# Optimization experiments

Measured on AMD Instinct MI355X. Metric: run time of the kernel, lower is better.

Reference implementation:

```python
import jax, jax.numpy as jnp
import numpy as np

V, S, D, H, L = 32000, 2048, 768, 12, 6
HD = D // H
EPS = 1e-5


def _sinusoidal_pe(s, d):
    pos = np.arange(s)[:, None].astype(np.float32)
    div = np.exp(np.arange(0, d, 2).astype(np.float32) * (-np.log(10000.0) / d))
    pe = np.zeros((s, d), dtype=np.float32)
    pe[:, 0::2] = np.sin(pos * div)
    pe[:, 1::2] = np.cos(pos * div)
    return jnp.asarray(pe)


def setup_inputs() -> dict:
    key = jax.random.key(0)
    ks = jax.random.split(key, 16)
    std = 0.02
    tok_emb = jax.random.normal(ks[0], (V, D), jnp.float32) * std
    tok_emb = tok_emb.at[1].set(0.0)  # padding_idx=1
    pos_enc = _sinusoidal_pe(S, D)
    attn_w = jax.random.normal(ks[1], (L, 3 * D, D), jnp.float32) * std
    attn_b = jnp.zeros((L, 3 * D), jnp.float32)
    proj_std = 0.02 / np.sqrt(2 * 6)
    proj_w = jax.random.normal(ks[2], (L, D, D), jnp.float32) * proj_std
    proj_b = jnp.zeros((L, D), jnp.float32)
    ln1_g = jnp.ones((L, D), jnp.float32); ln1_b = jnp.zeros((L, D), jnp.float32)
    ln2_g = jnp.ones((L, D), jnp.float32); ln2_b = jnp.zeros((L, D), jnp.float32)
    fc1_w = jax.random.normal(ks[3], (L, 4 * D, D), jnp.float32) * std
    fc1_b = jnp.zeros((L, 4 * D), jnp.float32)
    fc2_w = jax.random.normal(ks[4], (L, D, 4 * D), jnp.float32) * std
    fc2_b = jnp.zeros((L, D), jnp.float32)
    dec_w = jax.random.normal(ks[5], (V, D), jnp.float32) * std
    idx = jax.random.randint(ks[6], (2, S), 0, V)
    return dict(idx=idx, tok_emb=tok_emb, pos_enc=pos_enc, attn_w=attn_w,
                attn_b=attn_b, proj_w=proj_w, proj_b=proj_b, ln1_g=ln1_g,
                ln1_b=ln1_b, ln2_g=ln2_g, ln2_b=ln2_b, fc1_w=fc1_w,
                fc1_b=fc1_b, fc2_w=fc2_w, fc2_b=fc2_b, dec_w=dec_w)


def _ln(x, g, b):
    mu = jnp.mean(x, -1, keepdims=True)
    var = jnp.mean(jnp.square(x - mu), -1, keepdims=True)
    return (x - mu) * jax.lax.rsqrt(var + EPS) * g + b


def _forward(idx, tok_emb, pos_enc, attn_w, attn_b, proj_w, proj_b,
             ln1_g, ln1_b, ln2_g, ln2_b, fc1_w, fc1_b, fc2_w, fc2_b, dec_w):
    b, s = idx.shape
    x = tok_emb[idx] + pos_enc[:s]  # [b,s,d]
    for l in range(L):
        h = _ln(x, ln1_g[l], ln1_b[l])
        qkv = h @ attn_w[l].T + attn_b[l]
        q, k, v = jnp.split(qkv, 3, axis=-1)
        q = q.reshape(b, s, H, HD).transpose(0, 2, 1, 3)
        k = k.reshape(b, s, H, HD).transpose(0, 2, 1, 3)
        v = v.reshape(b, s, H, HD).transpose(0, 2, 1, 3)
        att = jnp.einsum('bhqd,bhkd->bhqk', q, k) * (1.0 / np.sqrt(HD))
        att = jax.nn.softmax(att, axis=-1)  # no causal mask in source
        y = jnp.einsum('bhqk,bhkd->bhqd', att, v)
        y = y.transpose(0, 2, 1, 3).reshape(b, s, D)
        x = x + (y @ proj_w[l].T + proj_b[l])
        h = _ln(x, ln2_g[l], ln2_b[l])
        h = jax.nn.gelu(h @ fc1_w[l].T + fc1_b[l])
        x = x + (h @ fc2_w[l].T + fc2_b[l])
    return x @ dec_w.T  # [b,s,V]


def reference(idx, tok_emb, pos_enc, attn_w, attn_b, proj_w, proj_b,
              ln1_g, ln1_b, ln2_g, ln2_b, fc1_w, fc1_b, fc2_w, fc2_b, dec_w):
    return _forward(idx, tok_emb, pos_enc, attn_w, attn_b, proj_w, proj_b,
                    ln1_g, ln1_b, ln2_g, ln2_b, fc1_w, fc1_b, fc2_w, fc2_b, dec_w)
```

## Files before the change

kernel.cpp:

```cpp
#include <hip/hip_runtime.h>
#include <hip/hip_bf16.h>
#include <stdint.h>


typedef unsigned short u16;
typedef __attribute__((ext_vector_type(8))) __bf16 bf16x8;
typedef __attribute__((ext_vector_type(4))) float f32x4;
typedef __attribute__((ext_vector_type(4))) unsigned int u32x4;
typedef __attribute__((ext_vector_type(4))) unsigned short u16x4;
typedef __attribute__((ext_vector_type(8))) unsigned short u16x8;

#define MFMA16(a, b, c) __builtin_amdgcn_mfma_f32_16x16x32_bf16((a), (b), (c), 0, 0, 0)

__device__ __forceinline__ float b2f(u16 u) {
  union { unsigned int i; float f; } x; x.i = ((unsigned int)u) << 16; return x.f;
}
__device__ __forceinline__ u16 f2b(float f) {
  union { float f; unsigned int i; } x; x.f = f;
  unsigned int r = x.i + 0x7fffu + ((x.i >> 16) & 1u);
  return (u16)(r >> 16);
}
__device__ __forceinline__ unsigned int cvtpk(float lo, float hi) {
  unsigned int r;
  asm("v_cvt_pk_bf16_f32 %0, %1, %2" : "=v"(r) : "v"(lo), "v"(hi));
  return r;
}
__device__ __forceinline__ float gelu_f(float v) {
  const float t = 0.7978845608028654f * (v + 0.044715f * v * v * v);
  const float e = __expf(-2.f * fabsf(t));
  float th = (1.f - e) / (1.f + e);
  th = (t < 0.f) ? -th : th;
  return 0.5f * v * (1.f + th);
}
__device__ __forceinline__ void lds16(u16* l, const u16* g) {
  __builtin_amdgcn_global_load_lds(
      (const __attribute__((address_space(1))) unsigned int*)g,
      (__attribute__((address_space(3))) unsigned int*)l, 16, 0, 0);
}

__global__ __launch_bounds__(256) void conv5_kernel(
    const float* __restrict__ s0, u16* __restrict__ d0, int n0,
    const float* __restrict__ s1, u16* __restrict__ d1, int n1,
    const float* __restrict__ s2, u16* __restrict__ d2, int n2,
    const float* __restrict__ s3, u16* __restrict__ d3, int n3,
    const float* __restrict__ s4, u16* __restrict__ d4, int n4) {
  const float* src; u16* dst; int n8;
  switch (blockIdx.y) {
    case 0: src = s0; dst = d0; n8 = n0; break;
    case 1: src = s1; dst = d1; n8 = n1; break;
    case 2: src = s2; dst = d2; n8 = n2; break;
    case 3: src = s3; dst = d3; n8 = n3; break;
    default: src = s4; dst = d4; n8 = n4; break;
  }
  int i = blockIdx.x * 256 + threadIdx.x;
  const int stride = gridDim.x * 256;
  for (; i < n8; i += stride) {
    const f32x4 a = *(const f32x4*)&src[(size_t)i * 8];
    const f32x4 b = *(const f32x4*)&src[(size_t)i * 8 + 4];
    u16x8 p;
#pragma unroll
    for (int j = 0; j < 4; ++j) { p[j] = f2b(a[j]); p[4 + j] = f2b(b[j]); }
    *(u16x8*)&dst[(size_t)i * 8] = p;
  }
}

__global__ __launch_bounds__(256) void embed_kernel(
    const int* __restrict__ idx, const float* __restrict__ tok,
    const float* __restrict__ pos, float* __restrict__ x) {
  const int t = blockIdx.x;
  const int s = t & 2047;
  const int tid = threadIdx.x;
  const size_t to = (size_t)idx[t] * 768;
  const size_t po = (size_t)s * 768;
  float* xr = x + (size_t)t * 768;
#pragma unroll
  for (int i = 0; i < 3; ++i) {
    const int d = tid + i * 256;
    xr[d] = tok[to + d] + pos[po + d];
  }
}

__global__ __launch_bounds__(256) void ln_kernel(
    const float* __restrict__ x, const float* __restrict__ g,
    const float* __restrict__ b, u16* __restrict__ out) {
  const int w = threadIdx.x >> 6, lane = threadIdx.x & 63;
  const int row = blockIdx.x * 4 + w;
  const float* xr = x + (size_t)row * 768;
  f32x4 v[3];
#pragma unroll
  for (int i = 0; i < 3; ++i) v[i] = *(const f32x4*)&xr[i * 256 + lane * 4];
  float s = 0.f;
#pragma unroll
  for (int i = 0; i < 3; ++i)
#pragma unroll
    for (int j = 0; j < 4; ++j) s += v[i][j];
#pragma unroll
  for (int m = 1; m < 64; m <<= 1) s += __shfl_xor(s, m);
  const float mu = s * (1.f / 768.f);
  float q = 0.f;
#pragma unroll
  for (int i = 0; i < 3; ++i)
#pragma unroll
    for (int j = 0; j < 4; ++j) {
      const float d = v[i][j] - mu;
      q += d * d;
    }
#pragma unroll
  for (int m = 1; m < 64; m <<= 1) q += __shfl_xor(q, m);
  const float rs = rsqrtf(q * (1.f / 768.f) + 1e-5f);
  u16* orow = out + (size_t)row * 768;
#pragma unroll
  for (int i = 0; i < 3; ++i) {
    const f32x4 gg = *(const f32x4*)&g[i * 256 + lane * 4];
    const f32x4 bb = *(const f32x4*)&b[i * 256 + lane * 4];
    u16x4 o;
#pragma unroll
    for (int j = 0; j < 4; ++j) o[j] = f2b((v[i][j] - mu) * rs * gg[j] + bb[j]);
    *(u16x4*)&orow[i * 256 + lane * 4] = o;
  }
}

template <int MODE, int MFAST>
__global__ __launch_bounds__(256) void gemm_bb(
    const u16* __restrict__ A, const u16* __restrict__ B,
    const float* __restrict__ bias, u16* __restrict__ outb,
    float* __restrict__ outf, float* __restrict__ resid,
    u16* __restrict__ mirror, int N, int K) {
  __shared__ alignas(16) u16 As[2][128 * 64];
  __shared__ alignas(16) u16 Bs[2][128 * 64];
  const int tid = threadIdx.x;
  const int lane = tid & 63;
  const int w = tid >> 6;
  const int wr = (w >> 1) * 64;
  const int wc = (w & 1) * 64;
  const int fr = lane & 15;
  const int fg = lane >> 4;
  const int bn0 = (MFAST ? blockIdx.y : blockIdx.x) * 128;
  const int bm0 = (MFAST ? blockIdx.x : blockIdx.y) * 128;
  const int srow = tid >> 3;

  f32x4 acc[4][4] = {};

  auto stage = [&](int buf, int bk0) {
#pragma unroll
    for (int i = 0; i < 4; ++i) {
      const int row = i * 32 + srow;
      const int slot = (tid & 7) ^ (row & 7);
      lds16(&As[buf][(i * 256 + w * 64) * 8],
            &A[(size_t)(bm0 + row) * K + bk0 + slot * 8]);
      lds16(&Bs[buf][(i * 256 + w * 64) * 8],
            &B[(size_t)(bn0 + row) * K + bk0 + slot * 8]);
    }
  };

  stage(0, 0);
  int cur = 0;
  for (int bk0 = 0; bk0 < K; bk0 += 64) {
    __syncthreads();
    if (bk0 + 64 < K) stage(cur ^ 1, bk0 + 64);
#pragma unroll
    for (int kk = 0; kk < 64; kk += 32) {
      bf16x8 af[4], bfv[4];
#pragma unroll
      for (int m = 0; m < 4; ++m) {
        const int row = wr + m * 16 + fr;
        const int slot = ((kk >> 3) + fg) ^ (row & 7);
        af[m] = *(const bf16x8*)&As[cur][row * 64 + slot * 8];
      }
#pragma unroll
      for (int n = 0; n < 4; ++n) {
        const int row = wc + n * 16 + fr;
        const int slot = ((kk >> 3) + fg) ^ (row & 7);
        bfv[n] = *(const bf16x8*)&Bs[cur][row * 64 + slot * 8];
      }
#pragma unroll
      for (int m = 0; m < 4; ++m)
#pragma unroll
        for (int n = 0; n < 4; ++n)
          acc[m][n] = MFMA16(af[m], bfv[n], acc[m][n]);
    }
    cur ^= 1;
  }

  if (MODE == 4 && bn0 >= 1536) {
#pragma unroll
    for (int n = 0; n < 4; ++n) {
      const int col = bn0 + wc + n * 16 + fr;
      const float bv = bias[col];
      const int hcol = col - 1536;
      const size_t vbase =
          (size_t)(hcol >> 6) * 64 * 2048 + (size_t)(hcol & 63) * 2048;
#pragma unroll
      for (int m = 0; m < 4; ++m) {
        const int row0 = bm0 + wr + m * 16 + fg * 4;
        const size_t bboff = (size_t)(row0 >> 11) * 12 * 64 * 2048;
        const int s = row0 & 2047;
        u16x4 o;
#pragma unroll
        for (int r = 0; r < 4; ++r) o[r] = f2b(acc[m][n][r] + bv);
        *(u16x4*)&mirror[bboff + vbase + s] = o;
      }
    }
    return;
  }

#pragma unroll
  for (int n = 0; n < 4; ++n) {
    const int col = bn0 + wc + n * 16 + fr;
    const float bv = bias ? bias[col] : 0.0f;
#pragma unroll
    for (int m = 0; m < 4; ++m) {
#pragma unroll
      for (int r = 0; r < 4; ++r) {
        const int row = bm0 + wr + m * 16 + fg * 4 + r;
        float v = acc[m][n][r] + bv;
        if (MODE == 1) v = gelu_f(v);
        const size_t off = (size_t)row * N + col;
        if (MODE == 2) {
          const float nv = resid[off] + v;
          resid[off] = nv;
          if (mirror) mirror[off] = f2b(nv);
        } else if (MODE == 3) {
          __builtin_nontemporal_store(v, &outf[off]);
        } else {
          outb[off] = f2b(v);
        }
      }
    }
  }
}

#define G8PHASE(H, MH, LOADB)                                                 \
  {                                                                           \
    if (LOADB) {                                                              \
      _Pragma("unroll") for (int n = 0; n < 4; ++n) {                         \
        const int row = wn * 64 + n * 16 + fr;                                \
        bfv[n] = *(const bf16x8*)&Bs_[bufr * 16384 + (H) * 8192 + row * 32 +  \
                                      ((fg ^ ((row ^ (row >> 2)) & 3)) << 3)];\
      }                                                                       \
    }                                                                         \
    bf16x8 af[4];                                                             \
    _Pragma("unroll") for (int m = 0; m < 4; ++m) {                           \
      const int row = wm * 128 + (MH) * 64 + m * 16 + fr;                     \
      af[m] = *(const bf16x8*)&As_[bufr * 16384 + (H) * 8192 + row * 32 +     \
                                   ((fg ^ ((row ^ (row >> 2)) & 3)) << 3)];   \
    }                                                                         \
    __builtin_amdgcn_s_setprio(1);                                            \
    _Pragma("unroll") for (int m = 0; m < 4; ++m)                             \
      _Pragma("unroll") for (int n = 0; n < 4; ++n)                           \
        acc[(MH) * 4 + m][n] = MFMA16(af[m], bfv[n], acc[(MH) * 4 + m][n]);   \
    __builtin_amdgcn_s_setprio(0);                                            \
  }

template <int MODE, int MFAST>
__global__ __launch_bounds__(512, 2) void gemm8(
    const u16* __restrict__ A, const u16* __restrict__ B,
    const float* __restrict__ bias, u16* __restrict__ outb,
    float* __restrict__ outf, float* __restrict__ resid, int N, int K) {
  extern __shared__ u16 sm8[];
  u16* As_ = sm8;
  u16* Bs_ = sm8 + 32768;
  const int tid = threadIdx.x;
  const int lane = tid & 63;
  const int w = tid >> 6;
  const int wm = w >> 2;
  const int wn = w & 3;
  const int fr = lane & 15;
  const int fg = lane >> 4;
  const int bn0 = (MFAST ? blockIdx.y : blockIdx.x) * 256;
  const int bm0 = (MFAST ? blockIdx.x : blockIdx.y) * 256;
  const int nt = K >> 6;

  f32x4 acc[8][4] = {};
  bf16x8 bfv[4];

  auto stage = [&](u16* lbase, const u16* __restrict__ M, int rbase, int k0) {
#pragma unroll
    for (int i = 0; i < 2; ++i) {
      const int c = i * 512 + tid;
      const int row = c >> 2;
      const int slot = (c & 3) ^ ((row ^ (row >> 2)) & 3);
      lds16(lbase + (i * 512 + w * 64) * 8,
            M + (size_t)(rbase + row) * K + k0 + slot * 8);
    }
  };

  stage(As_ + 0, A, bm0, 0);
  stage(Bs_ + 0, B, bn0, 0);
  stage(As_ + 8192, A, bm0, 32);
  stage(Bs_ + 8192, B, bn0, 32);

  int bufr = 0;
  for (int t = 0; t < nt; ++t) {
    const int tn = (t + 1 < nt) ? t + 1 : t;
    const int bufw = bufr ^ 1;
    const int kn = tn * 64;
    asm volatile("s_waitcnt vmcnt(4)" ::: "memory");
    __builtin_amdgcn_sched_barrier(0);
    __builtin_amdgcn_s_barrier();
    stage(As_ + bufw * 16384, A, bm0, kn);
    G8PHASE(0, 0, true)
    stage(Bs_ + bufw * 16384, B, bn0, kn);
    G8PHASE(0, 1, false)
    asm volatile("s_waitcnt vmcnt(4)" ::: "memory");
    __builtin_amdgcn_sched_barrier(0);
    __builtin_amdgcn_s_barrier();
    stage(As_ + bufw * 16384 + 8192, A, bm0, kn + 32);
    G8PHASE(1, 0, true)
    stage(Bs_ + bufw * 16384 + 8192, B, bn0, kn + 32);
    G8PHASE(1, 1, false)
    bufr ^= 1;
  }

#pragma unroll
  for (int n = 0; n < 4; ++n) {
    const int col = bn0 + wn * 64 + n * 16 + fr;
    const float bv = bias ? bias[col] : 0.0f;
#pragma unroll
    for (int i = 0; i < 8; ++i) {
#pragma unroll
      for (int r = 0; r < 4; ++r) {
        const int row = bm0 + wm * 128 + i * 16 + fg * 4 + r;
        float v = acc[i][n][r] + bv;
        if (MODE == 1) v = gelu_f(v);
        const size_t off = (size_t)row * N + col;
        if (MODE == 2) {
          resid[off] += v;
        } else if (MODE == 3) {
          __builtin_nontemporal_store(v, &outf[off]);
        } else {
          outb[off] = f2b(v);
        }
      }
    }
  }
}

template <int MODE>
__global__ __launch_bounds__(256) void gemm_bt(
    const u16* __restrict__ A, const float* __restrict__ B,
    const float* __restrict__ bias, u16* __restrict__ outb,
    float* __restrict__ outf, float* __restrict__ resid,
    u16* __restrict__ mirror, int N, int K) {
  __shared__ alignas(16) u16 As[128 * 64];
  __shared__ alignas(16) u16 Bs[128 * 64];
  const int tid = threadIdx.x;
  const int lane = tid & 63;
  const int w = tid >> 6;
  const int wr = (w >> 1) * 64;
  const int wc = (w & 1) * 64;
  const int fr = lane & 15;
  const int fg = lane >> 4;
  const int bn0 = blockIdx.x * 128;
  const int bm0 = blockIdx.y * 128;

  f32x4 acc[4][4] = {};

  for (int bk0 = 0; bk0 < K; bk0 += 64) {
    __syncthreads();
#pragma unroll
    for (int i = 0; i < 4; ++i) {
      const int c = i * 256 + tid;
      const int row = c >> 3;
      const int e0 = (c & 7) * 8;
      *(u32x4*)&As[row * 64 + e0] =
          *(const u32x4*)&A[(size_t)(bm0 + row) * K + bk0 + e0];
    }
#pragma unroll
    for (int i = 0; i < 8; ++i) {
      const int c = i * 256 + tid;
      const int row = c >> 4;
      const int e0 = (c & 15) * 4;
      const f32x4 fv = *(const f32x4*)&B[(size_t)(bn0 + row) * K + bk0 + e0];
      u16x4 pv;
#pragma unroll
      for (int j = 0; j < 4; ++j) pv[j] = f2b(fv[j]);
      *(u16x4*)&Bs[row * 64 + e0] = pv;
    }
    __syncthreads();
#pragma unroll
    for (int kk = 0; kk < 64; kk += 32) {
      bf16x8 af[4], bfv[4];
#pragma unroll
      for (int m = 0; m < 4; ++m)
        af[m] = *(const bf16x8*)&As[(wr + m * 16 + fr) * 64 + kk + fg * 8];
#pragma unroll
      for (int n = 0; n < 4; ++n)
        bfv[n] = *(const bf16x8*)&Bs[(wc + n * 16 + fr) * 64 + kk + fg * 8];
#pragma unroll
      for (int m = 0; m < 4; ++m)
#pragma unroll
        for (int n = 0; n < 4; ++n)
          acc[m][n] = MFMA16(af[m], bfv[n], acc[m][n]);
    }
  }

#pragma unroll
  for (int n = 0; n < 4; ++n) {
    const int col = bn0 + wc + n * 16 + fr;
    const float bv = bias ? bias[col] : 0.0f;
#pragma unroll
    for (int m = 0; m < 4; ++m) {
#pragma unroll
      for (int r = 0; r < 4; ++r) {
        const int row = bm0 + wr + m * 16 + fg * 4 + r;
        float v = acc[m][n][r] + bv;
        if (MODE == 1) v = gelu_f(v);
        const size_t off = (size_t)row * N + col;
        if (MODE == 2) {
          const float nv = resid[off] + v;
          resid[off] = nv;
          if (mirror) mirror[off] = f2b(nv);
        } else if (MODE == 3) {
          __builtin_nontemporal_store(v, &outf[off]);
        } else {
          outb[off] = f2b(v);
        }
      }
    }
  }
}

__global__ __launch_bounds__(256) void vtrans_kernel(
    const u16* __restrict__ qkv, u16* __restrict__ vt) {
  __shared__ u16 tile[64][72];
  const int tid = threadIdx.x;
  const int s0 = blockIdx.x * 64;
  const int hh = blockIdx.y;
  const int bb = blockIdx.z;
  const size_t tb = (size_t)bb * 2048 * 2304;
#pragma unroll
  for (int i = 0; i < 2; ++i) {
    const int c = i * 256 + tid;
    const int sl = c >> 3;
    const int d0 = (c & 7) * 8;
    *(u16x8*)&tile[sl][d0] =
        *(const u16x8*)&qkv[tb + (size_t)(s0 + sl) * 2304 + 1536 + hh * 64 + d0];
  }
  __syncthreads();
  const size_t vtb = (size_t)((bb * 12 + hh) * 64) * 2048;
#pragma unroll
  for (int i = 0; i < 2; ++i) {
    const int c = i * 256 + tid;
    const int d = c >> 3;
    const int so = (c & 7) * 8;
    u16x8 p;
#pragma unroll
    for (int j = 0; j < 8; ++j) p[j] = tile[so + j][d];
    *(u16x8*)&vt[vtb + (size_t)d * 2048 + s0 + so] = p;
  }
}

__global__ __launch_bounds__(256) void attn_kernel(
    const u16* __restrict__ qkv, const u16* __restrict__ vt,
    u16* __restrict__ y) {
  __shared__ alignas(16) u16 Ks[2][64 * 64];
  __shared__ alignas(16) u16 VTs[2][64 * 64];
  __shared__ alignas(16) u16 Ps[4][16 * 64];
  const int tid = threadIdx.x;
  const int lane = tid & 63;
  const int w = tid >> 6;
  const int fr = lane & 15;
  const int fg = lane >> 4;
  const int hh = blockIdx.y;
  const int bb = blockIdx.z;
  const size_t tb = (size_t)bb * 2048 * 2304;
  const size_t vtb = (size_t)((bb * 12 + hh) * 64) * 2048;
  const int q0 = blockIdx.x * 64 + w * 16;

  const bf16x8 qf0 =
      *(const bf16x8*)&qkv[tb + (size_t)(q0 + fr) * 2304 + hh * 64 + fg * 8];
  const bf16x8 qf1 =
      *(const bf16x8*)&qkv[tb + (size_t)(q0 + fr) * 2304 + hh * 64 + 32 + fg * 8];

  f32x4 oacc[4] = {};
  float m = -INFINITY, l = 0.f;

  const int chunkrow = lane >> 3;
  const int chunkslot = lane & 7;

  auto stage = [&](int buf, int kt) {
#pragma unroll
    for (int i = 0; i < 2; ++i) {
      const int row = (i * 4 + w) * 8 + chunkrow;
      const int slot = chunkslot ^ (row & 7);
      lds16(&Ks[buf][(i * 4 + w) * 512],
            &qkv[tb + (size_t)(kt + row) * 2304 + 768 + hh * 64 + slot * 8]);
      lds16(&VTs[buf][(i * 4 + w) * 512],
            &vt[vtb + (size_t)row * 2048 + kt + slot * 8]);
    }
  };

  stage(0, 0);
  int cur = 0;
  for (int kt = 0; kt < 2048; kt += 64) {
    __syncthreads();
    if (kt + 64 < 2048) stage(cur ^ 1, kt + 64);

    f32x4 s[4] = {};
#pragma unroll
    for (int kb = 0; kb < 4; ++kb) {
      const int row = kb * 16 + fr;
      const int sl0 = (fg) ^ (row & 7);
      const int sl1 = (4 + fg) ^ (row & 7);
      const bf16x8 k0 = *(const bf16x8*)&Ks[cur][row * 64 + sl0 * 8];
      const bf16x8 k1 = *(const bf16x8*)&Ks[cur][row * 64 + sl1 * 8];
      s[kb] = MFMA16(k0, qf0, s[kb]);
      s[kb] = MFMA16(k1, qf1, s[kb]);
    }

    float v[4][4];
    float mx = -INFINITY;
#pragma unroll
    for (int kb = 0; kb < 4; ++kb)
#pragma unroll
      for (int r = 0; r < 4; ++r) {
        v[kb][r] = s[kb][r] * 0.125f;
        mx = fmaxf(mx, v[kb][r]);
      }
    mx = fmaxf(mx, __shfl_xor(mx, 16));
    mx = fmaxf(mx, __shfl_xor(mx, 32));

    float alpha = 1.f;
    const bool resc = !__all(mx <= m);
    if (resc) {
      const float mn = fmaxf(m, mx);
      alpha = __expf(m - mn);
      m = mn;
    }

    float ps = 0.f;
    unsigned int pk[4][2];
#pragma unroll
    for (int kb = 0; kb < 4; ++kb) {
      const float p0 = __expf(v[kb][0] - m);
      const float p1 = __expf(v[kb][1] - m);
      const float p2 = __expf(v[kb][2] - m);
      const float p3 = __expf(v[kb][3] - m);
      ps += (p0 + p1) + (p2 + p3);
      pk[kb][0] = cvtpk(p0, p1);
      pk[kb][1] = cvtpk(p2, p3);
    }
    ps += __shfl_xor(ps, 16);
    ps += __shfl_xor(ps, 32);
    l = l * alpha + ps;

#pragma unroll
    for (int kb = 0; kb < 4; ++kb)
#pragma unroll
      for (int h = 0; h < 2; ++h) {
        const int off = fr * 64 + (((2 * kb + (fg >> 1)) ^ (fr & 7)) << 3) +
                        (2 * (fg & 1) + h) * 2;
        *(unsigned int*)&Ps[w][off] = pk[kb][h];
      }

    if (resc) {
      float alq[4];
#pragma unroll
      for (int r = 0; r < 4; ++r) alq[r] = __shfl(alpha, fg * 4 + r);
#pragma unroll
      for (int db = 0; db < 4; ++db)
#pragma unroll
        for (int r = 0; r < 4; ++r) oacc[db][r] *= alq[r];
    }

#pragma unroll
    for (int kh = 0; kh < 2; ++kh) {
      const bf16x8 pa =
          *(const bf16x8*)&Ps[w][fr * 64 + (((kh * 4 + fg) ^ (fr & 7)) << 3)];
#pragma unroll
      for (int db = 0; db < 4; ++db) {
        const int row = db * 16 + fr;
        const int slot = (kh * 4 + fg) ^ (row & 7);
        const bf16x8 vb = *(const bf16x8*)&VTs[cur][row * 64 + slot * 8];
        oacc[db] = MFMA16(pa, vb, oacc[db]);
      }
    }
    cur ^= 1;
  }

  float rq[4];
#pragma unroll
  for (int r = 0; r < 4; ++r) rq[r] = 1.0f / __shfl(l, fg * 4 + r);
#pragma unroll
  for (int db = 0; db < 4; ++db) {
#pragma unroll
    for (int r = 0; r < 4; ++r) {
      const int row = q0 + fg * 4 + r;
      y[(size_t)(bb * 2048 + row) * 768 + hh * 64 + db * 16 + fr] =
          f2b(oacc[db][r] * rq[r]);
    }
  }
}

extern "C" void kernel_launch(void* const* d_in, const int* in_sizes, int n_in,
                              void* d_out, int out_size, void* d_ws,
                              size_t ws_size, hipStream_t stream) {
  const int*   idx   = (const int*)d_in[0];
  const float* tok   = (const float*)d_in[1];
  const float* pos   = (const float*)d_in[2];
  const float* attnw = (const float*)d_in[3];
  const float* attnb = (const float*)d_in[4];
  const float* projw = (const float*)d_in[5];
  const float* projb = (const float*)d_in[6];
  const float* ln1g  = (const float*)d_in[7];
  const float* ln1b  = (const float*)d_in[8];
  const float* ln2g  = (const float*)d_in[9];
  const float* ln2b  = (const float*)d_in[10];
  const float* fc1w  = (const float*)d_in[11];
  const float* fc1b  = (const float*)d_in[12];
  const float* fc2w  = (const float*)d_in[13];
  const float* fc2b  = (const float*)d_in[14];
  const float* decw  = (const float*)d_in[15];

  char* ws = (char*)d_ws;
  float* x = (float*)(ws);
  u16* h   = (u16*)(ws + 12582912);
  u16* qkv = (u16*)(ws + 18874368);
  u16* y   = (u16*)(ws + 37748736);
  u16* h2  = (u16*)(ws + 18874368);

  const size_t WB0 = 44040192;
  u16* attnw_b = (u16*)(ws + WB0);
  u16* projw_b = (u16*)(ws + WB0 + 21233664);
  u16* fc1w_b  = (u16*)(ws + WB0 + 28311552);
  u16* fc2w_b  = (u16*)(ws + WB0 + 56623104);
  u16* decw_b  = (u16*)(ws + WB0 + 84934656);
  u16* vt      = (u16*)(ws + WB0 + 84934656 + 49152000);
  const size_t NEED = WB0 + 84934656 + 49152000 + 12582912;

  embed_kernel<<<4096, 256, 0, stream>>>(idx, tok, pos, x);

  if (ws_size >= NEED) {
    conv5_kernel<<<dim3(1024, 5), 256, 0, stream>>>(
        attnw, attnw_b, 10616832 / 8, projw, projw_b, 3538944 / 8, fc1w,
        fc1w_b, 14155776 / 8, fc2w, fc2w_b, 14155776 / 8, decw, decw_b,
        24576000 / 8);

    for (int l = 0; l < 6; ++l) {
      ln_kernel<<<1024, 256, 0, stream>>>(x, ln1g + l * 768, ln1b + l * 768, h);
      gemm_bb<4, 0><<<dim3(18, 32), 256, 0, stream>>>(
          h, attnw_b + (size_t)l * 2304 * 768, attnb + l * 2304, qkv, nullptr,
          nullptr, vt, 2304, 768);
      attn_kernel<<<dim3(32, 12, 2), 256, 0, stream>>>(qkv, vt, y);
      gemm_bb<2, 0><<<dim3(6, 32), 256, 0, stream>>>(
          y, projw_b + (size_t)l * 768 * 768, projb + l * 768, nullptr, nullptr,
          x, nullptr, 768, 768);
      ln_kernel<<<1024, 256, 0, stream>>>(x, ln2g + l * 768, ln2b + l * 768, h);
      gemm_bb<1, 0><<<dim3(24, 32), 256, 0, stream>>>(
          h, fc1w_b + (size_t)l * 3072 * 768, fc1b + l * 3072, h2, nullptr,
          nullptr, nullptr, 3072, 768);
      gemm_bb<2, 0><<<dim3(6, 32), 256, 0, stream>>>(
          h2, fc2w_b + (size_t)l * 768 * 3072, fc2b + l * 768, nullptr, nullptr,
          x, (l == 5) ? h : nullptr, 768, 3072);
    }
    gemm8<3, 1><<<dim3(16, 125), 512, 131072, stream>>>(
        h, decw_b, nullptr, nullptr, (float*)d_out, nullptr, 32000, 768);
  } else {
    for (int l = 0; l < 6; ++l) {
      ln_kernel<<<1024, 256, 0, stream>>>(x, ln1g + l * 768, ln1b + l * 768, h);
      gemm_bt<0><<<dim3(18, 32), 256, 0, stream>>>(
          h, attnw + (size_t)l * 2304 * 768, attnb + l * 2304, qkv, nullptr,
          nullptr, nullptr, 2304, 768);
      vtrans_kernel<<<dim3(32, 12, 2), 256, 0, stream>>>(qkv, (u16*)(ws + 12582912));
      attn_kernel<<<dim3(32, 12, 2), 256, 0, stream>>>(
          qkv, (u16*)(ws + 12582912), y);
      gemm_bt<2><<<dim3(6, 32), 256, 0, stream>>>(
          y, projw + (size_t)l * 768 * 768, projb + l * 768, nullptr, nullptr,
          x, nullptr, 768, 768);
      ln_kernel<<<1024, 256, 0, stream>>>(x, ln2g + l * 768, ln2b + l * 768, h);
      gemm_bt<1><<<dim3(24, 32), 256, 0, stream>>>(
          h, fc1w + (size_t)l * 3072 * 768, fc1b + l * 3072, h2, nullptr,
          nullptr, nullptr, 3072, 768);
      gemm_bt<2><<<dim3(6, 32), 256, 0, stream>>>(
          h2, fc2w + (size_t)l * 768 * 3072, fc2b + l * 768, nullptr, nullptr,
          x, (l == 5) ? h : nullptr, 768, 3072);
    }
    gemm_bt<3><<<dim3(250, 32), 256, 0, stream>>>(
        h, decw, nullptr, nullptr, (float*)d_out, nullptr, nullptr, 32000, 768);
  }
}
```

Before: 1.814 ms.

## Split-K the proj and fc2 GEMMs with atomic residual accumulation

Adds a SPLITK template parameter to the bf16 GEMM. The proj GEMM (K=768) now uses 2 K-slices and the fc2 GEMM (K=3072) uses 4, and each slice atomically adds its partial sum into the fp32 residual, with the bias applied only by slice 0. The aim is to fill the GPU better, since these N=768 GEMMs launched only 192 blocks. Because atomics cannot also write the bf16 mirror, a separate conversion kernel now produces the bf16 input for the final decoder GEMM. The cost is atomic traffic and summation order that is no longer deterministic.

```diff
diff --git a/kernel.cpp b/kernel.cpp
--- a/kernel.cpp
+++ b/kernel.cpp
@@ -64,6 +64,17 @@
   }
 }
 
+__global__ __launch_bounds__(256) void convh_kernel(
+    const float* __restrict__ src, u16* __restrict__ dst) {
+  const int i = blockIdx.x * 256 + threadIdx.x;
+  const f32x4 a = *(const f32x4*)&src[(size_t)i * 8];
+  const f32x4 b = *(const f32x4*)&src[(size_t)i * 8 + 4];
+  u16x8 p;
+#pragma unroll
+  for (int j = 0; j < 4; ++j) { p[j] = f2b(a[j]); p[4 + j] = f2b(b[j]); }
+  *(u16x8*)&dst[(size_t)i * 8] = p;
+}
+
 __global__ __launch_bounds__(256) void embed_kernel(
     const int* __restrict__ idx, const float* __restrict__ tok,
     const float* __restrict__ pos, float* __restrict__ x) {
@@ -120,7 +131,7 @@
   }
 }
 
-template <int MODE, int MFAST>
+template <int MODE, int MFAST, int SPLITK>
 __global__ __launch_bounds__(256) void gemm_bb(
     const u16* __restrict__ A, const u16* __restrict__ B,
     const float* __restrict__ bias, u16* __restrict__ outb,
@@ -138,6 +149,9 @@
   const int bn0 = (MFAST ? blockIdx.y : blockIdx.x) * 128;
   const int bm0 = (MFAST ? blockIdx.x : blockIdx.y) * 128;
   const int srow = tid >> 3;
+  const int kseg = K / SPLITK;
+  const int kbeg = (SPLITK > 1) ? blockIdx.z * kseg : 0;
+  const int kend = kbeg + kseg;
 
   f32x4 acc[4][4] = {};
 
@@ -153,11 +167,11 @@
     }
   };
 
-  stage(0, 0);
+  stage(0, kbeg);
   int cur = 0;
-  for (int bk0 = 0; bk0 < K; bk0 += 64) {
+  for (int bk0 = kbeg; bk0 < kend; bk0 += 64) {
     __syncthreads();
-    if (bk0 + 64 < K) stage(cur ^ 1, bk0 + 64);
+    if (bk0 + 64 < kend) stage(cur ^ 1, bk0 + 64);
 #pragma unroll
     for (int kk = 0; kk < 64; kk += 32) {
       bf16x8 af[4], bfv[4];
@@ -207,7 +221,8 @@
 #pragma unroll
   for (int n = 0; n < 4; ++n) {
     const int col = bn0 + wc + n * 16 + fr;
-    const float bv = bias ? bias[col] : 0.0f;
+    const float bv =
+        (bias && (SPLITK == 1 || blockIdx.z == 0)) ? bias[col] : 0.0f;
 #pragma unroll
     for (int m = 0; m < 4; ++m) {
 #pragma unroll
@@ -220,6 +235,8 @@
           const float nv = resid[off] + v;
           resid[off] = nv;
           if (mirror) mirror[off] = f2b(nv);
+        } else if (MODE == 5) {
+          atomicAdd(&resid[off], v);
         } else if (MODE == 3) {
           __builtin_nontemporal_store(v, &outf[off]);
         } else {
@@ -639,21 +656,22 @@
 
     for (int l = 0; l < 6; ++l) {
       ln_kernel<<<1024, 256, 0, stream>>>(x, ln1g + l * 768, ln1b + l * 768, h);
-      gemm_bb<4, 0><<<dim3(18, 32), 256, 0, stream>>>(
+      gemm_bb<4, 0, 1><<<dim3(18, 32), 256, 0, stream>>>(
           h, attnw_b + (size_t)l * 2304 * 768, attnb + l * 2304, qkv, nullptr,
           nullptr, vt, 2304, 768);
       attn_kernel<<<dim3(32, 12, 2), 256, 0, stream>>>(qkv, vt, y);
-      gemm_bb<2, 0><<<dim3(6, 32), 256, 0, stream>>>(
+      gemm_bb<5, 0, 2><<<dim3(6, 32, 2), 256, 0, stream>>>(
           y, projw_b + (size_t)l * 768 * 768, projb + l * 768, nullptr, nullptr,
           x, nullptr, 768, 768);
       ln_kernel<<<1024, 256, 0, stream>>>(x, ln2g + l * 768, ln2b + l * 768, h);
-      gemm_bb<1, 0><<<dim3(24, 32), 256, 0, stream>>>(
+      gemm_bb<1, 0, 1><<<dim3(24, 32), 256, 0, stream>>>(
           h, fc1w_b + (size_t)l * 3072 * 768, fc1b + l * 3072, h2, nullptr,
           nullptr, nullptr, 3072, 768);
-      gemm_bb<2, 0><<<dim3(6, 32), 256, 0, stream>>>(
+      gemm_bb<5, 0, 4><<<dim3(6, 32, 4), 256, 0, stream>>>(
           h2, fc2w_b + (size_t)l * 768 * 3072, fc2b + l * 768, nullptr, nullptr,
-          x, (l == 5) ? h : nullptr, 768, 3072);
-    }
+          x, nullptr, 768, 3072);
+    }
+    convh_kernel<<<1536, 256, 0, stream>>>(x, h);
     gemm8<3, 1><<<dim3(16, 125), 512, 131072, stream>>>(
         h, decw_b, nullptr, nullptr, (float*)d_out, nullptr, 32000, 768);
   } else {
@@ -662,7 +680,8 @@
       gemm_bt<0><<<dim3(18, 32), 256, 0, stream>>>(
           h, attnw + (size_t)l * 2304 * 768, attnb + l * 2304, qkv, nullptr,
           nullptr, nullptr, 2304, 768);
-      vtrans_kernel<<<dim3(32, 12, 2), 256, 0, stream>>>(qkv, (u16*)(ws + 12582912));
+      vtrans_kernel<<<dim3(32, 12, 2), 256, 0, stream>>>(
+          qkv, (u16*)(ws + 12582912));
       attn_kernel<<<dim3(32, 12, 2), 256, 0, stream>>>(
           qkv, (u16*)(ws + 12582912), y);
       gemm_bt<2><<<dim3(6, 32), 256, 0, stream>>>(
```

After: 1.761 ms. -2.9%, faster.
